# Kernel tuning notes

Measured on AMD Instinct MI355X. Metric: run time of the kernel, lower is better.

The kernel has to match this reference:

```python
import jax, jax.numpy as jnp
import numpy as np

B, CIN, MID, COUT, H, W = 4, 256, 128, 64, 128, 128
WS, HEADS = 8, 8
HD = MID // HEADS          # head dim = 16
N = WS * WS                # tokens per window = 64


def conv2d(x, w, pad=0, groups=1):
    return jax.lax.conv_general_dilated(
        x, w, (1, 1), ((pad, pad), (pad, pad)),
        feature_group_count=groups,
        dimension_numbers=('NCHW', 'OIHW', 'NCHW'))


def bn(x, g, b):  # eval-mode BatchNorm folded to per-channel affine
    return x * g[None, :, None, None] + b[None, :, None, None]


def setup_inputs() -> dict:
    key = jax.random.key(0)
    ks = jax.random.split(key, 32)
    nrm = lambda i, sh, s: jax.random.normal(ks[i], sh, jnp.float32) * s
    return {
        'x': nrm(0, (B, CIN, H, W), 1.0),
        'conv_w': nrm(1, (MID, CIN, 3, 3), 0.03),
        'bn1_g': 1.0 + nrm(2, (MID,), 0.05), 'bn1_b': nrm(3, (MID,), 0.05),
        'qkv_w': nrm(4, (3 * MID, MID, 1, 1), 0.05),
        'loc1_w': nrm(5, (MID, MID, 3, 3), 0.03),
        'loc1_g': 1.0 + nrm(6, (MID,), 0.05), 'loc1_b': nrm(7, (MID,), 0.05),
        'loc2_w': nrm(8, (MID, MID, 1, 1), 0.05),
        'loc2_g': 1.0 + nrm(9, (MID,), 0.05), 'loc2_b': nrm(10, (MID,), 0.05),
        'rel_table': nrm(11, ((2 * WS - 1) ** 2, HEADS), 0.02),
        'cw_w': nrm(12, (1, 2, 7, 7), 0.1),
        'cw_g': 1.0 + nrm(13, (1,), 0.05), 'cw_b': nrm(14, (1,), 0.05),
        'hc_w': nrm(15, (1, 2, 7, 7), 0.1),
        'hc_g': 1.0 + nrm(16, (1,), 0.05), 'hc_b': nrm(17, (1,), 0.05),
        'hw_w': nrm(18, (1, 2, 7, 7), 0.1),
        'hw_g': 1.0 + nrm(19, (1,), 0.05), 'hw_b': nrm(20, (1,), 0.05),
        'proj_dw': nrm(21, (MID, 1, WS, WS), 0.05),
        'proj_g': 1.0 + nrm(22, (MID,), 0.05), 'proj_b': nrm(23, (MID,), 0.05),
        'proj_pw': nrm(24, (MID, MID, 1, 1), 0.05),
        'up_w': nrm(25, (COUT, MID, 3, 3), 0.03),
    }


def _rel_pos_index():
    coords = np.stack(np.meshgrid(np.arange(WS), np.arange(WS), indexing='ij')).reshape(2, -1)
    rel = (coords[:, :, None] - coords[:, None, :]).transpose(1, 2, 0) + (WS - 1)
    return (rel[:, :, 0] * (2 * WS - 1) + rel[:, :, 1]).reshape(-1)  # [N*N]


def reference(x, conv_w, bn1_g, bn1_b, qkv_w, loc1_w, loc1_g, loc1_b,
              loc2_w, loc2_g, loc2_b, rel_table, cw_w, cw_g, cw_b,
              hc_w, hc_g, hc_b, hw_w, hw_g, hw_b,
              proj_dw, proj_g, proj_b, proj_pw, up_w):
    # DecoderBlock: conv -> BN -> ReLU
    h = jax.nn.relu(bn(conv2d(x, conv_w, pad=1), bn1_g, bn1_b))  # [B,MID,H,W]

    # GlobalLocalAttention
    local = bn(conv2d(h, loc2_w), loc2_g, loc2_b) + bn(conv2d(h, loc1_w, pad=1), loc1_g, loc1_b)

    # windowed qkv (H,W divisible by WS, no pad needed)
    hh, ww = H // WS, W // WS
    qkv = conv2d(h, qkv_w)  # [B, 3*MID, H, W]
    qkv = qkv.reshape(B, 3, HEADS, HD, hh, WS, ww, WS)
    qkv = qkv.transpose(1, 0, 4, 6, 2, 5, 7, 3).reshape(3, B * hh * ww, HEADS, N, HD)
    q, k, v = qkv[0], qkv[1], qkv[2]

    dots = jnp.einsum('bhnd,bhmd->bhnm', q, k) * (HD ** -0.5)  # [Bw,HEADS,N,N]
    bias = rel_table[jnp.asarray(_rel_pos_index())].reshape(N, N, HEADS).transpose(2, 0, 1)
    dots = dots + bias[None]

    # TripletAttention on dots treated as (B', C'=HEADS, H'=N, W'=N)
    def gate(t, w, g, b):
        z = jnp.concatenate([t.max(1, keepdims=True), t.mean(1, keepdims=True)], 1)  # ZPool
        return t * jax.nn.sigmoid(bn(conv2d(z, w, pad=3), g, b))

    d1 = gate(dots.transpose(0, 2, 1, 3), cw_w, cw_g, cw_b).transpose(0, 2, 1, 3)
    d2 = gate(dots.transpose(0, 3, 2, 1), hc_w, hc_g, hc_b).transpose(0, 3, 2, 1)
    d3 = gate(dots, hw_w, hw_g, hw_b)
    dots = (d1 + d2 + d3) / 3.0

    attn = jax.nn.softmax(dots, axis=-1)
    o = jnp.einsum('bhnm,bhmd->bhnd', attn, v)
    o = o.reshape(B, hh, ww, HEADS, WS, WS, HD).transpose(0, 3, 6, 1, 4, 2, 5).reshape(B, MID, H, W)

    # avg+max pooled sigmoid gates (kernel==stride==WS//2, exact reshape pooling)
    kp = WS // 2
    aw = o.reshape(B, MID, H // kp, kp, W)
    Fw = jax.nn.sigmoid(aw.mean(3) + aw.max(3))          # [B,MID,H/4,W]
    ah = o.reshape(B, MID, H, W // kp, kp)
    Fh = jax.nn.sigmoid(ah.mean(4) + ah.max(4))          # [B,MID,H,W/4]
    gmat = jnp.einsum('bchk,bckw->bchw', Fh, Fw)         # [B,MID,H,W]

    out = o * gmat + local
    out = jnp.pad(out, ((0, 0), (0, 0), (0, 1), (0, 1)), mode='reflect')  # pad_out
    # SeparableConvBN proj: depthwise k=WS pad=3 -> BN -> 1x1
    out = conv2d(out, proj_dw, pad=3, groups=MID)
    out = conv2d(bn(out, proj_g, proj_b), proj_pw)
    out = out[:, :, :H, :W]

    # upsample: ConvTranspose2d(k=3, s=2, p=1, op=1) as dilated conv
    up = jax.lax.conv_general_dilated(
        out, up_w, (1, 1), ((1, 2), (1, 2)), lhs_dilation=(2, 2),
        dimension_numbers=('NCHW', 'OIHW', 'NCHW'))  # [B,COUT,2H,2W]
    return up
```

## Files before the change

### kernel.cpp

```cpp
#include <hip/hip_runtime.h>
#include <hip/hip_bf16.h>

typedef __hip_bfloat16 bf16;
typedef __attribute__((ext_vector_type(8))) short short8;
typedef __attribute__((ext_vector_type(4))) float f32x4;

#define DEV __device__ __forceinline__
DEV float b2f(bf16 v){ return __bfloat162float(v); }
DEV bf16 f2b(float v){ return __float2bfloat16(v); }
DEV short f2bs(float v){ union{ bf16 b; short s; } u; u.b = __float2bfloat16(v); return u.s; }
DEV float sigm(float x){ return 1.f/(1.f + expf(-x)); }

#define BB 4
#define CIN 256
#define MID 128
#define COUT 64
#define HH 128
#define WW 128
#define WS 8
#define HEADS 8
#define HD 16
#define NTOK 64
#define NWIN 1024

static const size_t OFF_H     = 0;
static const size_t OFF_LOCAL = 33554432;
static const size_t OFF_Q     = 67108864;
static const size_t OFF_K     = 83886080;
static const size_t OFF_V     = 100663296;
static const size_t OFF_DOTS  = 117440512;
static const size_t OFF_Z1    = 184549376;
static const size_t OFF_Z2    = 186646528;
static const size_t OFF_Z3    = 188743680;
static const size_t OFF_G1    = 205520896;
static const size_t OFF_G2    = 207618048;
static const size_t OFF_G3    = 209715200;
static const size_t OFF_HT    = OFF_DOTS + 34078720;

__global__ __launch_bounds__(256) void k_wrep(const float* __restrict__ w, short* __restrict__ w2){
  int i = blockIdx.x*256 + threadIdx.x;
  int ci = i & 255, co = (i >> 8) & 127, kk = i >> 15;
  w2[i] = f2bs(w[(co*256 + ci)*9 + kk]);
}

__global__ void k_xzero(short* __restrict__ xT){
  int t = blockIdx.x*256 + threadIdx.x;
  int ci = t & 255, side = (t >> 8) & 1, row = t >> 9;
  int cpad = side ? 129 : 0;
  xT[((size_t)row*130 + cpad)*256 + ci] = 0;
}

__global__ __launch_bounds__(256) void k_xrep(const float* __restrict__ x, short* __restrict__ xT){
  const int blk = blockIdx.x;
  const int cgrp = blk & 1, cig = (blk >> 1) & 7, r = (blk >> 4) & 127, b = blk >> 11;
  const int c0 = cgrp*64, ci0 = cig*32;
  __shared__ float lds[32][65];
  const int t = threadIdx.x;
  for (int i = t; i < 2048; i += 256){
    int lci = i >> 6, c = i & 63;
    lds[lci][c] = x[((size_t)(b*256 + ci0 + lci)*128 + r)*128 + c0 + c];
  }
  __syncthreads();
  for (int i = t; i < 2048; i += 256){
    int lci = i & 31, cc = i >> 5;
    xT[((size_t)(b*128 + r)*130 + c0 + cc + 1)*256 + ci0 + lci] = f2bs(lds[lci][cc]);
  }
}

__global__ __launch_bounds__(256) void k_conv1m(const short* __restrict__ xT, const short* __restrict__ w2,
      const float* __restrict__ gg, const float* __restrict__ bb, float* __restrict__ h){
  const int blk = blockIdx.x;
  const int b = blk >> 7, y = blk & 127;
  const int t = threadIdx.x, lane = t & 63, wave = t >> 6;
  const int quad = lane >> 4, l15 = lane & 15;
  const int m0 = (wave >> 1)*64, n0 = (wave & 1)*64;
  __shared__ short as[130][32];
  __shared__ short bs[384][32];
  f32x4 acc[4][4];
  #pragma unroll
  for (int i = 0; i < 4; ++i)
    #pragma unroll
    for (int j = 0; j < 4; ++j) acc[i][j] = (f32x4){0.f,0.f,0.f,0.f};
  for (int ky = 0; ky < 3; ++ky){
    int r = y + ky - 1;
    if ((unsigned)r >= 128u) continue;
    const short* xrow = xT + (size_t)(b*128 + r)*130*256;
    const short* wk   = w2 + (size_t)ky*384*256;
    for (int ch = 0; ch < 8; ++ch){
      const int ci0 = ch*32;
      __syncthreads();
      for (int i = t; i < 520; i += 256){
        int col = i >> 2, cg = i & 3;
        *(uint4*)&as[col][cg*8] = *(const uint4*)&xrow[col*256 + ci0 + cg*8];
      }
      for (int i = t; i < 1536; i += 256){
        int rr = i >> 2, cg = i & 3;
        *(uint4*)&bs[rr][cg*8] = *(const uint4*)&wk[rr*256 + ci0 + cg*8];
      }
      __syncthreads();
      #pragma unroll
      for (int kx = 0; kx < 3; ++kx){
        short8 af[4], bf[4];
        #pragma unroll
        for (int mt = 0; mt < 4; ++mt)
          af[mt] = *(const short8*)&as[m0 + mt*16 + l15 + kx][quad*8];
        #pragma unroll
        for (int nt = 0; nt < 4; ++nt)
          bf[nt] = *(const short8*)&bs[kx*128 + n0 + nt*16 + l15][quad*8];
        #pragma unroll
        for (int mt = 0; mt < 4; ++mt)
          #pragma unroll
          for (int nt = 0; nt < 4; ++nt)
            acc[mt][nt] = __builtin_amdgcn_mfma_f32_16x16x32_bf16(af[mt], bf[nt], acc[mt][nt], 0, 0, 0);
      }
    }
  }
  #pragma unroll
  for (int nt = 0; nt < 4; ++nt){
    int co = n0 + nt*16 + l15;
    float g = gg[co], bia = bb[co];
    #pragma unroll
    for (int mt = 0; mt < 4; ++mt){
      int xb = m0 + mt*16 + quad*4;
      float4 o4;
      o4.x = fmaxf(acc[mt][nt][0]*g + bia, 0.f);
      o4.y = fmaxf(acc[mt][nt][1]*g + bia, 0.f);
      o4.z = fmaxf(acc[mt][nt][2]*g + bia, 0.f);
      o4.w = fmaxf(acc[mt][nt][3]*g + bia, 0.f);
      *(float4*)&h[((size_t)(b*128 + co)*128 + y)*128 + xb] = o4;
    }
  }
}

__global__ void k_hzero(short* __restrict__ hT){
  int t = blockIdx.x*256 + threadIdx.x;
  int ci = t & 127, side = (t >> 7) & 1, row = t >> 8;
  int cpad = side ? 129 : 0;
  hT[((size_t)row*130 + cpad)*128 + ci] = 0;
}

__global__ __launch_bounds__(256) void k_hrep(const float* __restrict__ h, short* __restrict__ hT){
  const int blk = blockIdx.x;
  const int cgrp = blk & 1, cig = (blk >> 1) & 3, r = (blk >> 3) & 127, b = blk >> 10;
  const int c0 = cgrp*64, ci0 = cig*32;
  __shared__ float lds[32][65];
  const int t = threadIdx.x;
  for (int i = t; i < 2048; i += 256){
    int lci = i >> 6, c = i & 63;
    lds[lci][c] = h[((size_t)(b*128 + ci0 + lci)*128 + r)*128 + c0 + c];
  }
  __syncthreads();
  for (int i = t; i < 2048; i += 256){
    int lci = i & 31, cc = i >> 5;
    hT[((size_t)(b*128 + r)*130 + c0 + cc + 1)*128 + ci0 + lci] = f2bs(lds[lci][cc]);
  }
}

__global__ __launch_bounds__(256) void k_lwrep(const float* __restrict__ w1, const float* __restrict__ g1,
      const float* __restrict__ w2, const float* __restrict__ g2, short* __restrict__ wloc){
  int i = blockIdx.x*256 + threadIdx.x;
  int ci = i & 127, row = (i >> 7) % 384, ky = i / 49152;
  int kx = row >> 7, co = row & 127;
  float v = w1[(co*128 + ci)*9 + ky*3 + kx] * g1[co];
  if (ky == 1 && kx == 1) v += w2[co*128 + ci] * g2[co];
  wloc[i] = f2bs(v);
}

__global__ __launch_bounds__(256) void k_localm(const short* __restrict__ hT, const short* __restrict__ wloc,
      const float* __restrict__ b1, const float* __restrict__ b2, float* __restrict__ out){
  const int blk = blockIdx.x;
  const int b = blk >> 7, y = blk & 127;
  const int t = threadIdx.x, lane = t & 63, wave = t >> 6;
  const int quad = lane >> 4, l15 = lane & 15;
  const int m0 = (wave >> 1)*64, n0 = (wave & 1)*64;
  __shared__ short as[130][32];
  __shared__ short bs[384][32];
  f32x4 acc[4][4];
  #pragma unroll
  for (int i = 0; i < 4; ++i)
    #pragma unroll
    for (int j = 0; j < 4; ++j) acc[i][j] = (f32x4){0.f,0.f,0.f,0.f};
  for (int ky = 0; ky < 3; ++ky){
    int r = y + ky - 1;
    if ((unsigned)r >= 128u) continue;
    const short* xrow = hT + (size_t)(b*128 + r)*130*128;
    const short* wk   = wloc + (size_t)ky*384*128;
    for (int ch = 0; ch < 4; ++ch){
      const int ci0 = ch*32;
      __syncthreads();
      for (int i = t; i < 520; i += 256){
        int col = i >> 2, cg = i & 3;
        *(uint4*)&as[col][cg*8] = *(const uint4*)&xrow[col*128 + ci0 + cg*8];
      }
      for (int i = t; i < 1536; i += 256){
        int rr = i >> 2, cg = i & 3;
        *(uint4*)&bs[rr][cg*8] = *(const uint4*)&wk[rr*128 + ci0 + cg*8];
      }
      __syncthreads();
      #pragma unroll
      for (int kx = 0; kx < 3; ++kx){
        short8 af[4], bf[4];
        #pragma unroll
        for (int mt = 0; mt < 4; ++mt)
          af[mt] = *(const short8*)&as[m0 + mt*16 + l15 + kx][quad*8];
        #pragma unroll
        for (int nt = 0; nt < 4; ++nt)
          bf[nt] = *(const short8*)&bs[kx*128 + n0 + nt*16 + l15][quad*8];
        #pragma unroll
        for (int mt = 0; mt < 4; ++mt)
          #pragma unroll
          for (int nt = 0; nt < 4; ++nt)
            acc[mt][nt] = __builtin_amdgcn_mfma_f32_16x16x32_bf16(af[mt], bf[nt], acc[mt][nt], 0, 0, 0);
      }
    }
  }
  #pragma unroll
  for (int nt = 0; nt < 4; ++nt){
    int co = n0 + nt*16 + l15;
    float bia = b1[co] + b2[co];
    #pragma unroll
    for (int mt = 0; mt < 4; ++mt){
      int xb = m0 + mt*16 + quad*4;
      float4 o4;
      o4.x = acc[mt][nt][0] + bia;
      o4.y = acc[mt][nt][1] + bia;
      o4.z = acc[mt][nt][2] + bia;
      o4.w = acc[mt][nt][3] + bia;
      *(float4*)&out[((size_t)(b*128 + co)*128 + y)*128 + xb] = o4;
    }
  }
}

__global__ __launch_bounds__(256) void k_wqkvrep(const float* __restrict__ w, short* __restrict__ wqkv){
  int i = blockIdx.x*256 + threadIdx.x;
  wqkv[i] = f2bs(w[i]);
}

__global__ __launch_bounds__(256) void k_qkvm(const short* __restrict__ hT, const short* __restrict__ wqkv,
      bf16* __restrict__ q, bf16* __restrict__ k, bf16* __restrict__ v){
  const int blk = blockIdx.x, ocg = blockIdx.y;
  const int b = blk >> 7, y = blk & 127;
  const int t = threadIdx.x, lane = t & 63, wave = t >> 6;
  const int quad = lane >> 4, l15 = lane & 15;
  const int m0 = (wave >> 1)*64, n0 = (wave & 1)*64;
  __shared__ short as[128][32];
  __shared__ short bs[128][32];
  const short* xrow = hT + ((size_t)(b*128 + y)*130 + 1)*128;
  const short* wk   = wqkv + (size_t)ocg*128*128;
  f32x4 acc[4][4];
  #pragma unroll
  for (int i = 0; i < 4; ++i)
    #pragma unroll
    for (int j = 0; j < 4; ++j) acc[i][j] = (f32x4){0.f,0.f,0.f,0.f};
  for (int ch = 0; ch < 4; ++ch){
    const int ci0 = ch*32;
    __syncthreads();
    for (int i = t; i < 512; i += 256){
      int col = i >> 2, cg = i & 3;
      *(uint4*)&as[col][cg*8] = *(const uint4*)&xrow[col*128 + ci0 + cg*8];
    }
    for (int i = t; i < 512; i += 256){
      int rr = i >> 2, cg = i & 3;
      *(uint4*)&bs[rr][cg*8] = *(const uint4*)&wk[rr*128 + ci0 + cg*8];
    }
    __syncthreads();
    short8 af[4], bf[4];
    #pragma unroll
    for (int mt = 0; mt < 4; ++mt)
      af[mt] = *(const short8*)&as[m0 + mt*16 + l15][quad*8];
    #pragma unroll
    for (int nt = 0; nt < 4; ++nt)
      bf[nt] = *(const short8*)&bs[n0 + nt*16 + l15][quad*8];
    #pragma unroll
    for (int mt = 0; mt < 4; ++mt)
      #pragma unroll
      for (int nt = 0; nt < 4; ++nt)
        acc[mt][nt] = __builtin_amdgcn_mfma_f32_16x16x32_bf16(af[mt], bf[nt], acc[mt][nt], 0, 0, 0);
  }
  bf16* dst = (ocg == 0) ? q : (ocg == 1) ? k : v;
  const int iy = y & 7, hy = y >> 3;
  #pragma unroll
  for (int nt = 0; nt < 4; ++nt){
    int co = n0 + nt*16 + l15;
    int head = co >> 4, d = co & 15;
    #pragma unroll
    for (int mt = 0; mt < 4; ++mt){
      int xb = m0 + mt*16 + quad*4;
      #pragma unroll
      for (int r = 0; r < 4; ++r){
        int x = xb + r;
        int bw = b*256 + hy*16 + (x >> 3);
        int n = iy*8 + (x & 7);
        dst[((size_t)(bw*8+head)*64 + n)*16 + d] = f2b(acc[mt][nt][r]);
      }
    }
  }
}

__global__ __launch_bounds__(256) void k_dots(const bf16* __restrict__ q, const bf16* __restrict__ kk,
      const float* __restrict__ rel, bf16* __restrict__ dots){
  const int bw = blockIdx.x, hd = blockIdx.y;
  __shared__ bf16 qs[64][16], ks[64][16];
  const int t = threadIdx.x;
  const size_t base = (size_t)(bw*8+hd)*1024;
  for (int i = t; i < 1024; i += 256){ qs[i>>4][i&15] = q[base + i]; ks[i>>4][i&15] = kk[base + i]; }
  __syncthreads();
  const int n = t >> 2, jm = t & 3;
  float qr[16];
  #pragma unroll
  for (int d = 0; d < 16; ++d) qr[d] = b2f(qs[n][d]);
  const int ny = n >> 3, nx = n & 7;
  for (int mm = 0; mm < 16; ++mm){
    int m = jm*16 + mm;
    float a = 0.f;
    #pragma unroll
    for (int d = 0; d < 16; ++d) a += qr[d]*b2f(ks[m][d]);
    int my = m >> 3, mx = m & 7;
    int ridx = (ny - my + 7)*15 + (nx - mx + 7);
    float bias = rel[ridx*8 + hd];
    dots[base*4 + (size_t)n*64 + m] = f2b(a*0.25f + bias);
  }
}

__global__ void k_z1(const bf16* __restrict__ dots, bf16* __restrict__ z){
  int t = blockIdx.x*256 + threadIdx.x;
  int bw = t >> 9, r = t & 511; int hd = r >> 6, m = r & 63;
  const bf16* p = dots + (size_t)(bw*8+hd)*4096 + m;
  float mx = -1e30f, sm = 0.f;
  for (int n = 0; n < 64; ++n){ float v = b2f(p[n*64]); mx = fmaxf(mx,v); sm += v; }
  z[(size_t)bw*1024 + hd*64 + m]       = f2b(mx);
  z[(size_t)bw*1024 + 512 + hd*64 + m] = f2b(sm*(1.f/64.f));
}
__global__ void k_z2(const bf16* __restrict__ dots, bf16* __restrict__ z){
  int t = blockIdx.x*256 + threadIdx.x;
  int bw = t >> 9, r = t & 511; int n = r >> 3, hd = r & 7;
  const bf16* p = dots + ((size_t)(bw*8+hd)*64 + n)*64;
  float mx = -1e30f, sm = 0.f;
  for (int m = 0; m < 64; ++m){ float v = b2f(p[m]); mx = fmaxf(mx,v); sm += v; }
  z[(size_t)bw*1024 + n*8 + hd]       = f2b(mx);
  z[(size_t)bw*1024 + 512 + n*8 + hd] = f2b(sm*(1.f/64.f));
}
__global__ void k_z3(const bf16* __restrict__ dots, bf16* __restrict__ z){
  int t = blockIdx.x*256 + threadIdx.x;
  int bw = t >> 12, r = t & 4095;
  const bf16* p = dots + (size_t)bw*32768 + r;
  float mx = -1e30f, sm = 0.f;
  for (int hd = 0; hd < 8; ++hd){ float v = b2f(p[hd*4096]); mx = fmaxf(mx,v); sm += v; }
  z[(size_t)bw*8192 + r]        = f2b(mx);
  z[(size_t)bw*8192 + 4096 + r] = f2b(sm*0.125f);
}

__global__ __launch_bounds__(256) void k_gate(const bf16* __restrict__ z, const float* __restrict__ w,
      const float* __restrict__ gg, const float* __restrict__ bb, float* __restrict__ G, int R, int C){
  __shared__ float wsm[98];
  const int t = threadIdx.x;
  if (t < 98) wsm[t] = w[t];
  __syncthreads();
  const int bw = blockIdx.x;
  int p = blockIdx.y*256 + t; if (p >= R*C) return;
  int y = p / C, x = p - y*C;
  float acc = 0.f;
  for (int c = 0; c < 2; ++c)
    for (int ky = 0; ky < 7; ++ky){
      int iy = y + ky - 3; if ((unsigned)iy >= (unsigned)R) continue;
      for (int kx = 0; kx < 7; ++kx){
        int ix = x + kx - 3; if ((unsigned)ix >= (unsigned)C) continue;
        acc += b2f(z[((size_t)(bw*2+c)*R + iy)*C + ix]) * wsm[c*49 + ky*7 + kx];
      }
    }
  G[(size_t)bw*R*C + p] = sigm(acc*gg[0] + bb[0]);
}

__global__ __launch_bounds__(256) void k_gate3(const bf16* __restrict__ z, const float* __restrict__ w,
      const float* __restrict__ gg, const float* __restrict__ bb, float* __restrict__ G){
  const int bw = blockIdx.x;
  __shared__ float pad[2][70][72];
  __shared__ float wsm[98];
  const int t = threadIdx.x;
  if (t < 98) wsm[t] = w[t];
  for (int i = t; i < 2*70*70; i += 256){
    int c = i / 4900, r = i % 4900;
    int py = r / 70, px = r % 70;
    int y = py - 3, x = px - 3;
    float v = 0.f;
    if ((unsigned)y < 64u && (unsigned)x < 64u)
      v = b2f(z[(size_t)bw*8192 + c*4096 + y*64 + x]);
    pad[c][py][px] = v;
  }
  __syncthreads();
  const int tx = t & 15, ty = t >> 4;
  const int x0 = tx*4, y0 = ty*4;
  float acc[4][4] = {};
  #pragma unroll
  for (int c = 0; c < 2; ++c){
    float wr[49];
    #pragma unroll
    for (int kk = 0; kk < 49; ++kk) wr[kk] = wsm[c*49 + kk];
    #pragma unroll
    for (int iy = 0; iy < 10; ++iy){
      float row[10];
      #pragma unroll
      for (int j = 0; j < 10; ++j) row[j] = pad[c][y0+iy][x0+j];
      #pragma unroll
      for (int dy = 0; dy < 4; ++dy){
        const int ky = iy - dy;
        if (ky < 0 || ky > 6) continue;
        #pragma unroll
        for (int kx = 0; kx < 7; ++kx){
          float wv = wr[ky*7 + kx];
          #pragma unroll
          for (int dx = 0; dx < 4; ++dx)
            acc[dy][dx] += wv * row[dx + kx];
        }
      }
    }
  }
  float g0 = gg[0], b0 = bb[0];
  #pragma unroll
  for (int dy = 0; dy < 4; ++dy){
    float4 o4;
    o4.x = sigm(acc[dy][0]*g0 + b0);
    o4.y = sigm(acc[dy][1]*g0 + b0);
    o4.z = sigm(acc[dy][2]*g0 + b0);
    o4.w = sigm(acc[dy][3]*g0 + b0);
    *(float4*)&G[(size_t)bw*4096 + (y0+dy)*64 + x0] = o4;
  }
}

__global__ __launch_bounds__(256) void k_attn(const bf16* __restrict__ dots, const float* __restrict__ G1,
      const float* __restrict__ G2, const float* __restrict__ G3, const bf16* __restrict__ v,
      float* __restrict__ o){
  const int bw = blockIdx.x, hd = blockIdx.y;
  const int b = bw >> 8, wy = (bw >> 4) & 15, wx = bw & 15;
  __shared__ float attn[64][65];
  __shared__ bf16 vs[64][16];
  __shared__ float invTot[64];
  const int t = threadIdx.x;
  for (int i = t; i < 1024; i += 256) vs[i>>4][i&15] = v[(size_t)(bw*8+hd)*1024 + i];
  const int n = t >> 2, j = t & 3;
  float g2v = G2[(size_t)bw*512 + n*8 + hd];
  const bf16* dp = dots + ((size_t)(bw*8+hd)*64 + n)*64 + j*16;
  const float* g1p = G1 + (size_t)bw*512 + hd*64 + j*16;
  const float* g3p = G3 + (size_t)bw*4096 + n*64 + j*16;
  float e[16]; float mx = -1e30f;
  #pragma unroll
  for (int m = 0; m < 16; ++m){
    float dv = b2f(dp[m]) * ((g1p[m] + g2v + g3p[m]) * (1.f/3.f));
    e[m] = dv; mx = fmaxf(mx, dv);
  }
  mx = fmaxf(mx, __shfl_xor(mx, 1, 4));
  mx = fmaxf(mx, __shfl_xor(mx, 2, 4));
  float s = 0.f;
  #pragma unroll
  for (int m = 0; m < 16; ++m){ float ev = expf(e[m]-mx); e[m] = ev; s += ev; }
  s += __shfl_xor(s, 1, 4);
  s += __shfl_xor(s, 2, 4);
  #pragma unroll
  for (int m = 0; m < 16; ++m) attn[n][j*16+m] = e[m];
  if (j == 0) invTot[n] = 1.f/s;
  __syncthreads();
  const int dg = j;
  float acc[4] = {0.f,0.f,0.f,0.f};
  for (int m = 0; m < 64; ++m){
    float a = attn[n][m];
    #pragma unroll
    for (int dd = 0; dd < 4; ++dd) acc[dd] += a * b2f(vs[m][dg*4+dd]);
  }
  float it = invTot[n];
  int y = wy*8 + (n>>3), x = wx*8 + (n&7);
  #pragma unroll
  for (int dd = 0; dd < 4; ++dd){
    int c = hd*16 + dg*4 + dd;
    o[((size_t)(b*128+c)*128 + y)*128 + x] = acc[dd]*it;
  }
}

__global__ void k_fw(const float* __restrict__ o, float* __restrict__ Fw){
  int t = blockIdx.x*256 + threadIdx.x; if (t >= 4*128*32*128) return;
  int x = t & 127, kk = (t>>7) & 31, bc = t >> 12;
  const float* p = o + ((size_t)bc*128 + kk*4)*128 + x;
  float mx = -1e30f, sm = 0.f;
  #pragma unroll
  for (int r = 0; r < 4; ++r){ float v = p[r*128]; mx = fmaxf(mx,v); sm += v; }
  Fw[t] = sigm(sm*0.25f + mx);
}
__global__ void k_fh(const float* __restrict__ o, float* __restrict__ Fh){
  int t = blockIdx.x*256 + threadIdx.x; if (t >= 4*128*128*32) return;
  int kk = t & 31, y = (t>>5) & 127, bc = t >> 12;
  const float* p = o + ((size_t)bc*128 + y)*128 + kk*4;
  float mx = -1e30f, sm = 0.f;
  #pragma unroll
  for (int r = 0; r < 4; ++r){ float v = p[r]; mx = fmaxf(mx,v); sm += v; }
  Fh[t] = sigm(sm*0.25f + mx);
}

__global__ __launch_bounds__(256) void k_comb(const float* __restrict__ o, const float* __restrict__ Fh,
      const float* __restrict__ Fw, const float* __restrict__ local, float* __restrict__ comb){
  const int bc = blockIdx.x;
  __shared__ float fh[128][33];
  __shared__ float fw[32][129];
  const int t = threadIdx.x;
  for (int i = t; i < 4096; i += 256) fh[i>>5][i&31]  = Fh[(size_t)bc*4096 + i];
  for (int i = t; i < 4096; i += 256) fw[i>>7][i&127] = Fw[(size_t)bc*4096 + i];
  __syncthreads();
  for (int i = t; i < 16384; i += 256){
    int y = i >> 7, x = i & 127;
    float g = 0.f;
    #pragma unroll
    for (int kk = 0; kk < 32; ++kk) g += fh[y][kk]*fw[kk][x];
    size_t idx = (size_t)bc*16384 + i;
    comb[idx] = o[idx]*g + local[idx];
  }
}

__global__ __launch_bounds__(256) void k_dw(const float* __restrict__ comb, const float* __restrict__ dw,
      const float* __restrict__ gg, const float* __restrict__ bb, float* __restrict__ out){
  const int tx = threadIdx.x, ty = threadIdx.y, t = ty*16+tx;
  const int bz = blockIdx.z; const int c = bz & 127;
  const int oy0 = blockIdx.y*16, ox0 = blockIdx.x*16;
  __shared__ float xs[23][23];
  __shared__ float wsm[64];
  if (t < 64) wsm[t] = dw[c*64 + t];
  for (int i = t; i < 529; i += 256){
    int iy = i/23, ix = i - iy*23;
    int y = oy0 + iy - 3, x = ox0 + ix - 3;
    float v = 0.f;
    if (y >= 0 && y <= 128 && x >= 0 && x <= 128){
      int yy = (y==128)?126:y, xx = (x==128)?126:x;
      v = comb[((size_t)bz*128 + yy)*128 + xx];
    }
    xs[iy][ix] = v;
  }
  __syncthreads();
  float acc = 0.f;
  #pragma unroll
  for (int ky = 0; ky < 8; ++ky)
    #pragma unroll
    for (int kx = 0; kx < 8; ++kx)
      acc += xs[ty+ky][tx+kx]*wsm[ky*8+kx];
  out[((size_t)bz*128 + oy0+ty)*128 + ox0+tx] = acc*gg[c] + bb[c];
}

__global__ void k_omzero(short* __restrict__ omT){
  int t = blockIdx.x*256 + threadIdx.x;
  int ci = t & 127, side = (t >> 7) & 1, row = t >> 8;
  int cpad = side ? 129 : 0;
  omT[((size_t)row*130 + cpad)*128 + ci] = 0;
}

__global__ __launch_bounds__(256) void k_uwrep(const float* __restrict__ w, short* __restrict__ wup){
  int i = blockIdx.x*256 + threadIdx.x;
  int ci = i & 127, co = (i >> 7) & 63, tap = i >> 13;
  wup[i] = f2bs(w[(co*128 + ci)*9 + tap]);
}

__global__ __launch_bounds__(256) void k_pw(const float* __restrict__ p1, const float* __restrict__ w,
      short* __restrict__ omT){
  const int pt = blockIdx.x, cb = blockIdx.y;
  const int P0 = pt*64; const int b = P0 >> 14; const int rem0 = P0 & 16383;
  const int y = rem0 >> 7, x0 = rem0 & 127;
  __shared__ float xsm[128][65];
  __shared__ float wsm[64][129];
  const int tx = threadIdx.x, ty = threadIdx.y, t = ty*16+tx;
  for (int i = t; i < 128*64; i += 256){
    int ci = i >> 6, p = i & 63;
    xsm[ci][p] = p1[(size_t)(b*128+ci)*16384 + rem0 + p];
  }
  for (int i = t; i < 64*128; i += 256){
    int co = i >> 7, ci = i & 127;
    wsm[co][ci] = w[(cb*64+co)*128 + ci];
  }
  __syncthreads();
  float acc[4][4] = {};
  for (int ci = 0; ci < 128; ++ci){
    float hv[4], wv[4];
    #pragma unroll
    for (int jj = 0; jj < 4; ++jj) hv[jj] = xsm[ci][jj*16+tx];
    #pragma unroll
    for (int ii = 0; ii < 4; ++ii) wv[ii] = wsm[ii*16+ty][ci];
    #pragma unroll
    for (int ii = 0; ii < 4; ++ii)
      #pragma unroll
      for (int jj = 0; jj < 4; ++jj) acc[ii][jj] += wv[ii]*hv[jj];
  }
  __syncthreads();
  float* pt_t = &xsm[0][0];
  #pragma unroll
  for (int ii = 0; ii < 4; ++ii)
    #pragma unroll
    for (int jj = 0; jj < 4; ++jj)
      pt_t[(jj*16+tx)*65 + ii*16+ty] = acc[ii][jj];
  __syncthreads();
  for (int i = t; i < 4096; i += 256){
    int px = i >> 6, co_l = i & 63;
    omT[((size_t)(b*128 + y)*130 + x0 + px + 1)*128 + cb*64 + co_l] = f2bs(pt_t[px*65 + co_l]);
  }
}

__global__ __launch_bounds__(256) void k_upm(const short* __restrict__ omT, const short* __restrict__ wup,
      float* __restrict__ out){
  const int blk = blockIdx.x;
  const int b = blk >> 7, y = blk & 127;
  const int t = threadIdx.x, lane = t & 63, wave = t >> 6;
  const int quad = lane >> 4, l15 = lane & 15;
  const int m0w = wave*32;
  __shared__ __align__(16) char smem[53504];
  short* asp = (short*)smem;
  short* bsp = (short*)(smem + 16640);
  float* ptile = (float*)smem;
  const int PAR[9] = {3,2,3, 1,0,1, 3,2,3};
  const int ROW[9] = {0,0,0, 0,0,0, 1,1,1};
  const int SHF[9] = {0,0,1, 0,0,1, 0,0,1};
  f32x4 acc[4][2][4];
  #pragma unroll
  for (int p = 0; p < 4; ++p)
    #pragma unroll
    for (int mt = 0; mt < 2; ++mt)
      #pragma unroll
      for (int nt = 0; nt < 4; ++nt) acc[p][mt][nt] = (f32x4){0.f,0.f,0.f,0.f};
  for (int ch = 0; ch < 4; ++ch){
    const int ci0 = ch*32;
    __syncthreads();
    for (int i = t; i < 1040; i += 256){
      int rw = (i >= 520), j = i - rw*520;
      int col = j >> 2, cg = j & 3;
      uint4 val = {0,0,0,0};
      if (y + rw < 128)
        val = *(const uint4*)&omT[((size_t)(b*128 + y + rw)*130 + col)*128 + ci0 + cg*8];
      *(uint4*)&asp[((rw*130 + col)*32) + cg*8] = val;
    }
    for (int i = t; i < 2304; i += 256){
      int rr = i >> 2, cg = i & 3;
      *(uint4*)&bsp[rr*32 + cg*8] = *(const uint4*)&wup[rr*128 + ci0 + cg*8];
    }
    __syncthreads();
    #pragma unroll
    for (int k = 0; k < 9; ++k){
      const int pr = PAR[k], rw = ROW[k], sh = SHF[k];
      if (rw && y == 127) continue;
      short8 af[2], bf[4];
      #pragma unroll
      for (int mt = 0; mt < 2; ++mt)
        af[mt] = *(const short8*)&asp[((rw*130 + m0w + mt*16 + l15 + 1 + sh))*32 + quad*8];
      #pragma unroll
      for (int nt = 0; nt < 4; ++nt)
        bf[nt] = *(const short8*)&bsp[(k*64 + nt*16 + l15)*32 + quad*8];
      #pragma unroll
      for (int mt = 0; mt < 2; ++mt)
        #pragma unroll
        for (int nt = 0; nt < 4; ++nt)
          acc[pr][mt][nt] = __builtin_amdgcn_mfma_f32_16x16x32_bf16(af[mt], bf[nt], acc[pr][mt][nt], 0, 0, 0);
    }
  }
  #pragma unroll
  for (int p = 0; p < 4; ++p){
    __syncthreads();
    #pragma unroll
    for (int mt = 0; mt < 2; ++mt)
      #pragma unroll
      for (int nt = 0; nt < 4; ++nt){
        int co = nt*16 + l15;
        int xb = m0w + mt*16 + quad*4;
        #pragma unroll
        for (int r = 0; r < 4; ++r)
          ptile[co*132 + xb + r] = acc[p][mt][nt][r];
      }
    __syncthreads();
    int py = p >> 1, px = p & 1;
    int Y = 2*y + py;
    for (int i = t; i < 8192; i += 256){
      int co = i >> 7, xx = i & 127;
      out[((size_t)(b*64 + co)*256 + Y)*256 + 2*xx + px] = ptile[co*132 + xx];
    }
  }
}

extern "C" void kernel_launch(void* const* d_in, const int* in_sizes, int n_in,
                              void* d_out, int out_size, void* d_ws, size_t ws_size,
                              hipStream_t stream) {
  const float* x       = (const float*)d_in[0];
  const float* conv_w  = (const float*)d_in[1];
  const float* bn1_g   = (const float*)d_in[2];
  const float* bn1_b   = (const float*)d_in[3];
  const float* qkv_w   = (const float*)d_in[4];
  const float* loc1_w  = (const float*)d_in[5];
  const float* loc1_g  = (const float*)d_in[6];
  const float* loc1_b  = (const float*)d_in[7];
  const float* loc2_w  = (const float*)d_in[8];
  const float* loc2_g  = (const float*)d_in[9];
  const float* loc2_b  = (const float*)d_in[10];
  const float* rel_t   = (const float*)d_in[11];
  const float* cw_w    = (const float*)d_in[12];
  const float* cw_g    = (const float*)d_in[13];
  const float* cw_b    = (const float*)d_in[14];
  const float* hc_w    = (const float*)d_in[15];
  const float* hc_g    = (const float*)d_in[16];
  const float* hc_b    = (const float*)d_in[17];
  const float* hw_w    = (const float*)d_in[18];
  const float* hw_g    = (const float*)d_in[19];
  const float* hw_b    = (const float*)d_in[20];
  const float* proj_dw = (const float*)d_in[21];
  const float* proj_g  = (const float*)d_in[22];
  const float* proj_b  = (const float*)d_in[23];
  const float* proj_pw = (const float*)d_in[24];
  const float* up_w    = (const float*)d_in[25];

  char* ws = (char*)d_ws;
  float* h      = (float*)(ws + OFF_H);
  float* local  = (float*)(ws + OFF_LOCAL);
  bf16*  q      = (bf16*)(ws + OFF_Q);
  bf16*  k      = (bf16*)(ws + OFF_K);
  bf16*  v      = (bf16*)(ws + OFF_V);
  bf16*  dots   = (bf16*)(ws + OFF_DOTS);
  bf16*  z1     = (bf16*)(ws + OFF_Z1);
  bf16*  z2     = (bf16*)(ws + OFF_Z2);
  bf16*  z3     = (bf16*)(ws + OFF_Z3);
  float* G1     = (float*)(ws + OFF_G1);
  float* G2     = (float*)(ws + OFF_G2);
  float* G3     = (float*)(ws + OFF_G3);
  short* xT     = (short*)(ws + OFF_DOTS);
  short* hT     = (short*)(ws + OFF_HT);
  short* w2bf   = (short*)(ws + OFF_Z1);
  short* wloc   = (short*)(ws + OFF_Z2);
  short* wqkv   = (short*)(ws + OFF_Z3);
  short* omT    = (short*)(ws + OFF_DOTS);
  short* wup    = (short*)(ws + OFF_Z1);
  float* o_img  = (float*)(ws + OFF_Q);
  float* Fh     = (float*)(ws + OFF_DOTS);
  float* Fw     = (float*)(ws + OFF_DOTS + 8388608);
  float* comb   = (float*)(ws + OFF_H);
  float* proj1  = (float*)(ws + OFF_LOCAL);
  float* outp   = (float*)d_out;

  dim3 blk2(16,16);
  k_wrep <<<1152, 256, 0, stream>>>(conv_w, w2bf);
  k_xzero<<<1024, 256, 0, stream>>>(xT);
  k_xrep <<<8192, 256, 0, stream>>>(x, xT);
  k_conv1m<<<512, 256, 0, stream>>>(xT, w2bf, bn1_g, bn1_b, h);
  k_lwrep<<<576, 256, 0, stream>>>(loc1_w, loc1_g, loc2_w, loc2_g, wloc);
  k_hzero<<<512, 256, 0, stream>>>(hT);
  k_hrep <<<4096, 256, 0, stream>>>(h, hT);
  k_localm<<<512, 256, 0, stream>>>(hT, wloc, loc1_b, loc2_b, local);
  k_wqkvrep<<<192, 256, 0, stream>>>(qkv_w, wqkv);
  k_qkvm <<<dim3(512,3), 256, 0, stream>>>(hT, wqkv, q, k, v);
  k_dots <<<dim3(NWIN,8), 256, 0, stream>>>(q, k, rel_t, dots);
  k_z1   <<<2048, 256, 0, stream>>>(dots, z1);
  k_z2   <<<2048, 256, 0, stream>>>(dots, z2);
  k_z3   <<<16384, 256, 0, stream>>>(dots, z3);
  k_gate <<<dim3(NWIN,2),  256, 0, stream>>>(z1, cw_w, cw_g, cw_b, G1, 8, 64);
  k_gate <<<dim3(NWIN,2),  256, 0, stream>>>(z2, hc_w, hc_g, hc_b, G2, 64, 8);
  k_gate3<<<NWIN, 256, 0, stream>>>(z3, hw_w, hw_g, hw_b, G3);
  k_attn <<<dim3(NWIN,8), 256, 0, stream>>>(dots, G1, G2, G3, v, o_img);
  k_fw   <<<8192, 256, 0, stream>>>(o_img, Fw);
  k_fh   <<<8192, 256, 0, stream>>>(o_img, Fh);
  k_comb <<<512, 256, 0, stream>>>(o_img, Fh, Fw, local, comb);
  k_dw   <<<dim3(8,8,BB*128), blk2, 0, stream>>>(comb, proj_dw, proj_g, proj_b, proj1);
  k_omzero<<<512, 256, 0, stream>>>(omT);
  k_uwrep<<<288, 256, 0, stream>>>(up_w, wup);
  k_pw   <<<dim3(1024,2), blk2, 0, stream>>>(proj1, proj_pw, omT);
  k_upm  <<<512, 256, 0, stream>>>(omT, wup, outp);
}
```

Baseline: 735.7 us.

## Register-tile depthwise 8x8 conv over full-width row strips

The depthwise projection conv now gives each block a 16-row strip across the full image width instead of a 16x16 tile. Each thread computes a 2x4 output micro-tile from float4 shared-memory row loads reused across kernel taps, and writes results with float4 stores. This cuts halo reloads and shared-memory reads per output. In exchange it raises register pressure and lowers the block count from 32768 to 4096.

```diff
diff --git a/kernel.cpp b/kernel.cpp
--- a/kernel.cpp
+++ b/kernel.cpp
@@ -515,30 +515,56 @@
 
 __global__ __launch_bounds__(256) void k_dw(const float* __restrict__ comb, const float* __restrict__ dw,
       const float* __restrict__ gg, const float* __restrict__ bb, float* __restrict__ out){
-  const int tx = threadIdx.x, ty = threadIdx.y, t = ty*16+tx;
-  const int bz = blockIdx.z; const int c = bz & 127;
-  const int oy0 = blockIdx.y*16, ox0 = blockIdx.x*16;
-  __shared__ float xs[23][23];
+  const int bz = blockIdx.y;
+  const int oy0 = blockIdx.x*16;
+  const int c = bz & 127;
+  __shared__ float xs[23][136];
   __shared__ float wsm[64];
+  const int t = threadIdx.x;
   if (t < 64) wsm[t] = dw[c*64 + t];
-  for (int i = t; i < 529; i += 256){
-    int iy = i/23, ix = i - iy*23;
-    int y = oy0 + iy - 3, x = ox0 + ix - 3;
+  for (int i = t; i < 23*135; i += 256){
+    int py = i / 135, px = i - py*135;
+    int gy = oy0 + py - 3, gx = px - 3;
     float v = 0.f;
-    if (y >= 0 && y <= 128 && x >= 0 && x <= 128){
-      int yy = (y==128)?126:y, xx = (x==128)?126:x;
+    if (gy >= 0 && gy <= 128 && gx >= 0 && gx <= 128){
+      int yy = (gy==128)?126:gy, xx = (gx==128)?126:gx;
       v = comb[((size_t)bz*128 + yy)*128 + xx];
     }
-    xs[iy][ix] = v;
-  }
-  __syncthreads();
-  float acc = 0.f;
-  #pragma unroll
-  for (int ky = 0; ky < 8; ++ky)
-    #pragma unroll
-    for (int kx = 0; kx < 8; ++kx)
-      acc += xs[ty+ky][tx+kx]*wsm[ky*8+kx];
-  out[((size_t)bz*128 + oy0+ty)*128 + ox0+tx] = acc*gg[c] + bb[c];
+    xs[py][px] = v;
+  }
+  __syncthreads();
+  const int tx = t & 31, ty = t >> 5;
+  const int x0 = tx*4, y0 = ty*2;
+  float acc[2][4] = {};
+  #pragma unroll
+  for (int iy = 0; iy < 9; ++iy){
+    float row[12];
+    *(float4*)&row[0] = *(const float4*)&xs[y0+iy][x0];
+    *(float4*)&row[4] = *(const float4*)&xs[y0+iy][x0+4];
+    *(float4*)&row[8] = *(const float4*)&xs[y0+iy][x0+8];
+    #pragma unroll
+    for (int dy = 0; dy < 2; ++dy){
+      const int ky = iy - dy;
+      if (ky < 0 || ky > 7) continue;
+      #pragma unroll
+      for (int kx = 0; kx < 8; ++kx){
+        float wv = wsm[ky*8 + kx];
+        #pragma unroll
+        for (int dx = 0; dx < 4; ++dx)
+          acc[dy][dx] += wv * row[dx + kx];
+      }
+    }
+  }
+  float g = gg[c], bi = bb[c];
+  #pragma unroll
+  for (int dy = 0; dy < 2; ++dy){
+    float4 o4;
+    o4.x = acc[dy][0]*g + bi;
+    o4.y = acc[dy][1]*g + bi;
+    o4.z = acc[dy][2]*g + bi;
+    o4.w = acc[dy][3]*g + bi;
+    *(float4*)&out[((size_t)bz*128 + oy0 + y0 + dy)*128 + x0] = o4;
+  }
 }
 
 __global__ void k_omzero(short* __restrict__ omT){
@@ -754,7 +780,7 @@
   k_fw   <<<8192, 256, 0, stream>>>(o_img, Fw);
   k_fh   <<<8192, 256, 0, stream>>>(o_img, Fh);
   k_comb <<<512, 256, 0, stream>>>(o_img, Fh, Fw, local, comb);
-  k_dw   <<<dim3(8,8,BB*128), blk2, 0, stream>>>(comb, proj_dw, proj_g, proj_b, proj1);
+  k_dw   <<<dim3(8, BB*128), 256, 0, stream>>>(comb, proj_dw, proj_g, proj_b, proj1);
   k_omzero<<<512, 256, 0, stream>>>(omT);
   k_uwrep<<<288, 256, 0, stream>>>(up_w, wup);
   k_pw   <<<dim3(1024,2), blk2, 0, stream>>>(proj1, proj_pw, omT);
```

Result: faster. 698.1 us (-5.1%).
